# Optimization experiments

Hardware: AMD Instinct MI355X
Metric: run time of the kernel (lower is better)

## Reference

```python
import jax, jax.numpy as jnp
import numpy as np

B, C, L = 128, 12, 1024
N_DIL, DIV, H, K, KSZ, NCP = 7, 2, 32, 8, 9, 6


def setup_inputs() -> dict:
    key = jax.random.key(0)
    kx, kw, ki = jax.random.split(key, 3)
    X = jax.random.normal(kx, (B, C, L), dtype=jnp.float32)
    W = jax.random.normal(kw, (N_DIL, DIV, K * H, 1, KSZ), dtype=jnp.float32)
    # Hydra weight normalization: zero mean, unit L1 norm along the kernel taps
    W = W - W.mean(-1, keepdims=True)
    W = W / jnp.abs(W).sum(-1, keepdims=True)
    I = jax.random.randint(ki, (N_DIL, DIV, H, NCP), 0, C, dtype=jnp.int32)
    return {"X": X, "W": W, "I": I}


def _forward(X, W, I):
    b = X.shape[0]
    diff_X = X[..., 1:] - X[..., :-1]  # first-order difference series
    bi = jnp.arange(b)[:, None, None]
    hi = jnp.arange(H)[None, :, None]
    Z = []
    for di in range(N_DIL):
        d = 2 ** di
        p = (KSZ - 1) * d // 2  # 'same' padding -> output length == input length
        for j in range(DIV):
            src = X if j == 0 else diff_X
            # irregular channel gather + sum over selected channels: [b, H, L']
            g = src[:, I[di, j]].sum(2)
            # grouped dilated conv1d: groups=H, k=K outputs per group -> [b, K*H, L']
            y = jax.lax.conv_general_dilated(
                g, W[di, j], window_strides=(1,), padding=[(p, p)],
                rhs_dilation=(d,), dimension_numbers=("NCH", "OIH", "NCH"),
                feature_group_count=H)
            y = y.reshape(b, H, K, -1)  # [b, H, K, L'] (group-major channel order)
            mx = y.max(2)               # [b, H, L']
            amx = y.argmax(2)
            amn = y.argmin(2)
            # scatter_add histograms over which kernel won at each position
            count_max = jnp.zeros((b, H, K), y.dtype).at[bi, hi, amx].add(mx)
            count_min = jnp.zeros((b, H, K), y.dtype).at[bi, hi, amn].add(jnp.ones_like(mx))
            Z.append(count_max)
            Z.append(count_min)
    return jnp.concatenate(Z, axis=1).reshape(b, -1)


def reference(X, W, I):
    return _forward(X, W, I)
```

## Files before the change

kernel.cpp:

```cpp
#include <hip/hip_runtime.h>

#define NB 128
#define NC 12
#define NL 1024
#define NDIL 7
#define NDIV 2
#define NH 32
#define NK 8
#define NKSZ 9
#define NNCP 6
#define OUTPB (NDIL*NDIV*2*NH*NK)

#define SER_STRIDE 1280
#define LDS_FLOATS (4*SER_STRIDE + 256)

__device__ __forceinline__ float4 ld4(const float* p) { return *(const float4*)p; }

__device__ __forceinline__ float sgpr_f(float v) {
    return __int_as_float(__builtin_amdgcn_readfirstlane(__float_as_int(v)));
}

template<int CTRL, int RM>
__device__ __forceinline__ float dppadd_f(float x) {
    int t = __builtin_amdgcn_update_dpp(0, __float_as_int(x), CTRL, RM, 0xf, false);
    return x + __int_as_float(t);
}
template<int CTRL, int RM>
__device__ __forceinline__ unsigned dppadd_u(unsigned x) {
    int t = __builtin_amdgcn_update_dpp(0, (int)x, CTRL, RM, 0xf, false);
    return x + (unsigned)t;
}
#define RSUM_F(x) { x = dppadd_f<0x111,0xf>(x); x = dppadd_f<0x112,0xf>(x); \
                    x = dppadd_f<0x114,0xf>(x); x = dppadd_f<0x118,0xf>(x); \
                    x = dppadd_f<0x142,0xa>(x); x = dppadd_f<0x143,0xc>(x); }
#define RSUM_U(x) { x = dppadd_u<0x111,0xf>(x); x = dppadd_u<0x112,0xf>(x); \
                    x = dppadd_u<0x114,0xf>(x); x = dppadd_u<0x118,0xf>(x); \
                    x = dppadd_u<0x142,0xa>(x); x = dppadd_u<0x143,0xc>(x); }

#define Wk(k,t) wf[(k)*NKSZ+(t)]

#define ARGBIN(A, OK)                                                     \
    {                                                                     \
        float mx = fmaxf(fmaxf(A[0], A[1]), A[2]);                        \
        mx = fmaxf(fmaxf(mx, A[3]), A[4]);                                \
        mx = fmaxf(fmaxf(mx, A[5]), A[6]);                                \
        mx = fmaxf(mx, A[7]);                                             \
        float mn = fminf(fminf(A[0], A[1]), A[2]);                        \
        mn = fminf(fminf(mn, A[3]), A[4]);                                \
        mn = fminf(fminf(mn, A[5]), A[6]);                                \
        mn = fminf(mn, A[7]);                                             \
        if (OK) {                                                         \
            _Pragma("unroll")                                             \
            for (int k = 0; k < NK; ++k) {                                \
                cm[k] += (A[k] == mx) ? A[k] : 0.f;                       \
                cn[k] += (A[k] == mn) ? 1u : 0u;                          \
            }                                                             \
        }                                                                 \
    }

template<int D>
__device__ __forceinline__ void conv_body(const float* __restrict__ bp0,
                                          const float (&wf)[NK*NKSZ], bool okl,
                                          float (&cm)[NK], unsigned (&cn)[NK]) {
    if constexpr (D == 1) {
        const float* bp = bp0 - 4;
        for (int c = 0; c < 8; ++c, bp += 128) {
            float2 q0 = *(const float2*)(bp);
            float2 q1 = *(const float2*)(bp + 2);
            float2 q2 = *(const float2*)(bp + 4);
            float2 q3 = *(const float2*)(bp + 6);
            float2 q4 = *(const float2*)(bp + 8);
            const float win[10] = { q0.x,q0.y,q1.x,q1.y,q2.x,q2.y,q3.x,q3.y,q4.x,q4.y };
            float a0[NK], a1[NK];
            #pragma unroll
            for (int k = 0; k < NK; ++k) { a0[k] = 0.f; a1[k] = 0.f; }
            #pragma unroll
            for (int t = 0; t < NKSZ; ++t)
                #pragma unroll
                for (int k = 0; k < NK; ++k) {
                    a0[k] = fmaf(Wk(k,t), win[t],   a0[k]);
                    a1[k] = fmaf(Wk(k,t), win[t+1], a1[k]);
                }
            ARGBIN(a0, true);
            ARGBIN(a1, (c != 7) || okl);
        }
    } else {
        const float* bp = bp0 - 4*D;
        for (int c = 0; c < 8; ++c, bp += 128) {
            float2 r[NKSZ];
            #pragma unroll
            for (int t = 0; t < NKSZ; ++t)
                r[t] = *(const float2*)(bp + t*D);
            float a0[NK], a1[NK];
            #pragma unroll
            for (int k = 0; k < NK; ++k) { a0[k] = 0.f; a1[k] = 0.f; }
            #pragma unroll
            for (int t = 0; t < NKSZ; ++t)
                #pragma unroll
                for (int k = 0; k < NK; ++k) {
                    a0[k] = fmaf(Wk(k,t), r[t].x, a0[k]);
                    a1[k] = fmaf(Wk(k,t), r[t].y, a1[k]);
                }
            ARGBIN(a0, true);
            ARGBIN(a1, (c != 7) || okl);
        }
    }
}

__global__ __launch_bounds__(256) void hydra_kernel(
    const float* __restrict__ X,
    const float* __restrict__ W,
    const int*   __restrict__ I,
    float*       __restrict__ out)
{
    __shared__ float lds[LDS_FLOATS];

    const int bid = blockIdx.x;
    const int h4 = bid & 7;
    const int dj = (bid >> 3) % 14;
    const int b  = (bid >> 3) / 14;
    const int di = dj >> 1;
    const int j  = dj & 1;

    const int tid  = threadIdx.x;
    const int lane = tid & 63;
    const int wid  = __builtin_amdgcn_readfirstlane(tid >> 6);
    const int h    = h4 * 4 + wid;
    const int Sw   = 256 + wid * SER_STRIDE;

    #pragma unroll
    for (int z = 0; z < 2; ++z) {
        float4 zz; zz.x = 0.f; zz.y = 0.f; zz.z = 0.f; zz.w = 0.f;
        *(float4*)(lds + (wid + z) * SER_STRIDE + 4 * lane) = zz;
    }

    const int* idx = I + ((di*NDIV + j)*NH + h)*NNCP;
    const float* xb = X + (size_t)b * NC * NL;
    const float* p0 = xb + idx[0]*NL;
    const float* p1 = xb + idx[1]*NL;
    const float* p2 = xb + idx[2]*NL;
    const float* p3 = xb + idx[3]*NL;
    const float* p4 = xb + idx[4]*NL;
    const float* p5 = xb + idx[5]*NL;

    if (j == 0) {
        #pragma unroll
        for (int c = 0; c < 4; ++c) {
            const int e = 256*c + 4*lane;
            float4 v0 = ld4(p0+e), v1 = ld4(p1+e), v2 = ld4(p2+e);
            float4 v3 = ld4(p3+e), v4 = ld4(p4+e), v5 = ld4(p5+e);
            float4 s;
            s.x = v0.x+v1.x+v2.x+v3.x+v4.x+v5.x;
            s.y = v0.y+v1.y+v2.y+v3.y+v4.y+v5.y;
            s.z = v0.z+v1.z+v2.z+v3.z+v4.z+v5.z;
            s.w = v0.w+v1.w+v2.w+v3.w+v4.w+v5.w;
            *(float4*)(lds + Sw + e) = s;
        }
    } else {
        float4 sa[4];
        #pragma unroll
        for (int c = 0; c < 4; ++c) {
            const int e = 256*c + 4*lane;
            float4 v0 = ld4(p0+e), v1 = ld4(p1+e), v2 = ld4(p2+e);
            float4 v3 = ld4(p3+e), v4 = ld4(p4+e), v5 = ld4(p5+e);
            sa[c].x = v0.x+v1.x+v2.x+v3.x+v4.x+v5.x;
            sa[c].y = v0.y+v1.y+v2.y+v3.y+v4.y+v5.y;
            sa[c].z = v0.z+v1.z+v2.z+v3.z+v4.z+v5.z;
            sa[c].w = v0.w+v1.w+v2.w+v3.w+v4.w+v5.w;
        }
        #pragma unroll
        for (int c = 0; c < 4; ++c) {
            const float nxt = (c < 3) ? __shfl(sa[(c+1) & 3].x, 0, 64) : 0.f;
            const float sh  = __shfl_down(sa[c].x, 1, 64);
            const float Se4 = (lane == 63) ? nxt : sh;
            float4 df;
            df.x = sa[c].y - sa[c].x;
            df.y = sa[c].z - sa[c].y;
            df.z = sa[c].w - sa[c].z;
            df.w = Se4 - sa[c].w;
            if (c == 3 && lane == 63) df.w = 0.f;
            const int e = 256*c + 4*lane;
            *(float4*)(lds + Sw + e) = df;
        }
    }

    float wf[NK*NKSZ];
    {
        const float* Wp = W + (size_t)((di*NDIV + j)*(NK*NH) + h*NK) * NKSZ;
        #pragma unroll
        for (int i = 0; i < 18; ++i) {
            float4 v = ld4(Wp + 4*i);
            wf[4*i+0] = sgpr_f(v.x); wf[4*i+1] = sgpr_f(v.y);
            wf[4*i+2] = sgpr_f(v.z); wf[4*i+3] = sgpr_f(v.w);
        }
    }

    float    cm[NK];
    unsigned cn[NK];
    #pragma unroll
    for (int k = 0; k < NK; ++k) { cm[k] = 0.f; cn[k] = 0u; }

    const float* bp0 = lds + Sw + 2*lane;
    const bool   okl = (j == 0) || (lane != 63);

    switch (di) {
        case 0: conv_body<1>( bp0, wf, okl, cm, cn); break;
        case 1: conv_body<2>( bp0, wf, okl, cm, cn); break;
        case 2: conv_body<4>( bp0, wf, okl, cm, cn); break;
        case 3: conv_body<8>( bp0, wf, okl, cm, cn); break;
        case 4: conv_body<16>(bp0, wf, okl, cm, cn); break;
        case 5: conv_body<32>(bp0, wf, okl, cm, cn); break;
        default: conv_body<64>(bp0, wf, okl, cm, cn); break;
    }

    unsigned cp[4];
    #pragma unroll
    for (int i = 0; i < 4; ++i) cp[i] = cn[2*i] | (cn[2*i+1] << 16);

    #pragma unroll
    for (int k = 0; k < NK; ++k) RSUM_F(cm[k]);
    #pragma unroll
    for (int i = 0; i < 4; ++i) RSUM_U(cp[i]);

    if (lane == 63) {
        float* ob = out + (size_t)b*OUTPB + (dj*2)*(NH*NK) + h*NK;
        #pragma unroll
        for (int k = 0; k < NK; ++k) ob[k] = cm[k];
        float* oc = ob + NH*NK;
        #pragma unroll
        for (int i = 0; i < 4; ++i) {
            oc[2*i]     = (float)(cp[i] & 0xffffu);
            oc[2*i + 1] = (float)(cp[i] >> 16);
        }
    }
}

extern "C" void kernel_launch(void* const* d_in, const int* in_sizes, int n_in,
                              void* d_out, int out_size, void* d_ws, size_t ws_size,
                              hipStream_t stream) {
    const float* X = (const float*)d_in[0];
    const float* W = (const float*)d_in[1];
    const int*   I = (const int*)d_in[2];
    float* out = (float*)d_out;

    const int nblocks = NB * (NDIL*NDIV) * (NH/4);
    hydra_kernel<<<dim3(nblocks), dim3(256), 0, stream>>>(X, W, I, out);
}
```

Baseline: 159.1 us.

## Store LDS series as packed fp16 and loop persistent blocks over work items

The gathered channel-sum and difference series are packed to fp16 with round-toward-zero when written to LDS and widened back to fp32 when read for the dilated convolution. This halves LDS footprint and read width. The grid becomes a fixed 2048 blocks, each looping over 7 work items, with a launch-bounds hint for 8 blocks per CU, to cut block launch overhead and raise occupancy. The cost is extra convert instructions. The reduced precision can also flip which kernel wins argmax/argmin, which changes the histogram counts relative to the fp32 reference.

```diff
diff --git a/kernel.cpp b/kernel.cpp
--- a/kernel.cpp
+++ b/kernel.cpp
@@ -11,13 +11,25 @@
 #define NNCP 6
 #define OUTPB (NDIL*NDIV*2*NH*NK)
 
-#define SER_STRIDE 1280
-#define LDS_FLOATS (4*SER_STRIDE + 256)
+#define SER16 1280
+#define LDS_F16 (4*SER16 + 256)
+
+#define GRID_BLOCKS 2048
+#define ITEMS_PER_BLOCK 7
+
+typedef __fp16 h2 __attribute__((ext_vector_type(2)));
 
 __device__ __forceinline__ float4 ld4(const float* p) { return *(const float4*)p; }
 
 __device__ __forceinline__ float sgpr_f(float v) {
     return __int_as_float(__builtin_amdgcn_readfirstlane(__float_as_int(v)));
+}
+__device__ __forceinline__ h2 pkrtz(float x, float y) {
+    return __builtin_amdgcn_cvt_pkrtz(x, y);
+}
+__device__ __forceinline__ float2 cvt2(unsigned u) {
+    h2 v = __builtin_bit_cast(h2, u);
+    float2 r; r.x = (float)v.x; r.y = (float)v.y; return r;
 }
 
 template<int CTRL, int RM>
@@ -59,17 +71,17 @@
     }
 
 template<int D>
-__device__ __forceinline__ void conv_body(const float* __restrict__ bp0,
+__device__ __forceinline__ void conv_body(const __fp16* __restrict__ bp0,
                                           const float (&wf)[NK*NKSZ], bool okl,
                                           float (&cm)[NK], unsigned (&cn)[NK]) {
     if constexpr (D == 1) {
-        const float* bp = bp0 - 4;
+        const __fp16* bp = bp0 - 4;
         for (int c = 0; c < 8; ++c, bp += 128) {
-            float2 q0 = *(const float2*)(bp);
-            float2 q1 = *(const float2*)(bp + 2);
-            float2 q2 = *(const float2*)(bp + 4);
-            float2 q3 = *(const float2*)(bp + 6);
-            float2 q4 = *(const float2*)(bp + 8);
+            float2 q0 = cvt2(*(const unsigned*)(bp));
+            float2 q1 = cvt2(*(const unsigned*)(bp + 2));
+            float2 q2 = cvt2(*(const unsigned*)(bp + 4));
+            float2 q3 = cvt2(*(const unsigned*)(bp + 6));
+            float2 q4 = cvt2(*(const unsigned*)(bp + 8));
             const float win[10] = { q0.x,q0.y,q1.x,q1.y,q2.x,q2.y,q3.x,q3.y,q4.x,q4.y };
             float a0[NK], a1[NK];
             #pragma unroll
@@ -85,12 +97,12 @@
             ARGBIN(a1, (c != 7) || okl);
         }
     } else {
-        const float* bp = bp0 - 4*D;
+        const __fp16* bp = bp0 - 4*D;
         for (int c = 0; c < 8; ++c, bp += 128) {
             float2 r[NKSZ];
             #pragma unroll
             for (int t = 0; t < NKSZ; ++t)
-                r[t] = *(const float2*)(bp + t*D);
+                r[t] = cvt2(*(const unsigned*)(bp + t*D));
             float a0[NK], a1[NK];
             #pragma unroll
             for (int k = 0; k < NK; ++k) { a0[k] = 0.f; a1[k] = 0.f; }
@@ -107,130 +119,139 @@
     }
 }
 
-__global__ __launch_bounds__(256) void hydra_kernel(
+__global__ __launch_bounds__(256, 8) void hydra_kernel(
     const float* __restrict__ X,
     const float* __restrict__ W,
     const int*   __restrict__ I,
     float*       __restrict__ out)
 {
-    __shared__ float lds[LDS_FLOATS];
-
-    const int bid = blockIdx.x;
-    const int h4 = bid & 7;
-    const int dj = (bid >> 3) % 14;
-    const int b  = (bid >> 3) / 14;
-    const int di = dj >> 1;
-    const int j  = dj & 1;
+    __shared__ __fp16 lds16[LDS_F16];
 
     const int tid  = threadIdx.x;
     const int lane = tid & 63;
     const int wid  = __builtin_amdgcn_readfirstlane(tid >> 6);
-    const int h    = h4 * 4 + wid;
-    const int Sw   = 256 + wid * SER_STRIDE;
+    const int Sw   = 256 + wid * SER16;
 
     #pragma unroll
     for (int z = 0; z < 2; ++z) {
-        float4 zz; zz.x = 0.f; zz.y = 0.f; zz.z = 0.f; zz.w = 0.f;
-        *(float4*)(lds + (wid + z) * SER_STRIDE + 4 * lane) = zz;
-    }
-
-    const int* idx = I + ((di*NDIV + j)*NH + h)*NNCP;
-    const float* xb = X + (size_t)b * NC * NL;
-    const float* p0 = xb + idx[0]*NL;
-    const float* p1 = xb + idx[1]*NL;
-    const float* p2 = xb + idx[2]*NL;
-    const float* p3 = xb + idx[3]*NL;
-    const float* p4 = xb + idx[4]*NL;
-    const float* p5 = xb + idx[5]*NL;
-
-    if (j == 0) {
-        #pragma unroll
-        for (int c = 0; c < 4; ++c) {
-            const int e = 256*c + 4*lane;
-            float4 v0 = ld4(p0+e), v1 = ld4(p1+e), v2 = ld4(p2+e);
-            float4 v3 = ld4(p3+e), v4 = ld4(p4+e), v5 = ld4(p5+e);
-            float4 s;
-            s.x = v0.x+v1.x+v2.x+v3.x+v4.x+v5.x;
-            s.y = v0.y+v1.y+v2.y+v3.y+v4.y+v5.y;
-            s.z = v0.z+v1.z+v2.z+v3.z+v4.z+v5.z;
-            s.w = v0.w+v1.w+v2.w+v3.w+v4.w+v5.w;
-            *(float4*)(lds + Sw + e) = s;
-        }
-    } else {
-        float4 sa[4];
-        #pragma unroll
-        for (int c = 0; c < 4; ++c) {
-            const int e = 256*c + 4*lane;
-            float4 v0 = ld4(p0+e), v1 = ld4(p1+e), v2 = ld4(p2+e);
-            float4 v3 = ld4(p3+e), v4 = ld4(p4+e), v5 = ld4(p5+e);
-            sa[c].x = v0.x+v1.x+v2.x+v3.x+v4.x+v5.x;
-            sa[c].y = v0.y+v1.y+v2.y+v3.y+v4.y+v5.y;
-            sa[c].z = v0.z+v1.z+v2.z+v3.z+v4.z+v5.z;
-            sa[c].w = v0.w+v1.w+v2.w+v3.w+v4.w+v5.w;
-        }
-        #pragma unroll
-        for (int c = 0; c < 4; ++c) {
-            const float nxt = (c < 3) ? __shfl(sa[(c+1) & 3].x, 0, 64) : 0.f;
-            const float sh  = __shfl_down(sa[c].x, 1, 64);
-            const float Se4 = (lane == 63) ? nxt : sh;
-            float4 df;
-            df.x = sa[c].y - sa[c].x;
-            df.y = sa[c].z - sa[c].y;
-            df.z = sa[c].w - sa[c].z;
-            df.w = Se4 - sa[c].w;
-            if (c == 3 && lane == 63) df.w = 0.f;
-            const int e = 256*c + 4*lane;
-            *(float4*)(lds + Sw + e) = df;
-        }
-    }
-
-    float wf[NK*NKSZ];
-    {
-        const float* Wp = W + (size_t)((di*NDIV + j)*(NK*NH) + h*NK) * NKSZ;
-        #pragma unroll
-        for (int i = 0; i < 18; ++i) {
-            float4 v = ld4(Wp + 4*i);
-            wf[4*i+0] = sgpr_f(v.x); wf[4*i+1] = sgpr_f(v.y);
-            wf[4*i+2] = sgpr_f(v.z); wf[4*i+3] = sgpr_f(v.w);
-        }
-    }
-
-    float    cm[NK];
-    unsigned cn[NK];
-    #pragma unroll
-    for (int k = 0; k < NK; ++k) { cm[k] = 0.f; cn[k] = 0u; }
-
-    const float* bp0 = lds + Sw + 2*lane;
-    const bool   okl = (j == 0) || (lane != 63);
-
-    switch (di) {
-        case 0: conv_body<1>( bp0, wf, okl, cm, cn); break;
-        case 1: conv_body<2>( bp0, wf, okl, cm, cn); break;
-        case 2: conv_body<4>( bp0, wf, okl, cm, cn); break;
-        case 3: conv_body<8>( bp0, wf, okl, cm, cn); break;
-        case 4: conv_body<16>(bp0, wf, okl, cm, cn); break;
-        case 5: conv_body<32>(bp0, wf, okl, cm, cn); break;
-        default: conv_body<64>(bp0, wf, okl, cm, cn); break;
-    }
-
-    unsigned cp[4];
-    #pragma unroll
-    for (int i = 0; i < 4; ++i) cp[i] = cn[2*i] | (cn[2*i+1] << 16);
-
-    #pragma unroll
-    for (int k = 0; k < NK; ++k) RSUM_F(cm[k]);
-    #pragma unroll
-    for (int i = 0; i < 4; ++i) RSUM_U(cp[i]);
-
-    if (lane == 63) {
-        float* ob = out + (size_t)b*OUTPB + (dj*2)*(NH*NK) + h*NK;
-        #pragma unroll
-        for (int k = 0; k < NK; ++k) ob[k] = cm[k];
-        float* oc = ob + NH*NK;
-        #pragma unroll
-        for (int i = 0; i < 4; ++i) {
-            oc[2*i]     = (float)(cp[i] & 0xffffu);
-            oc[2*i + 1] = (float)(cp[i] >> 16);
+        uint2 zz; zz.x = 0u; zz.y = 0u;
+        *(uint2*)(lds16 + (wid + z) * SER16 + 4 * lane) = zz;
+    }
+
+    #pragma unroll 1
+    for (int it = 0; it < ITEMS_PER_BLOCK; ++it) {
+        const int item = blockIdx.x + it * GRID_BLOCKS;
+        const int h4 = item & 7;
+        const int dj = (item >> 3) % 14;
+        const int b  = (item >> 3) / 14;
+        const int di = dj >> 1;
+        const int j  = dj & 1;
+        const int h  = h4 * 4 + wid;
+
+        const int* idx = I + ((di*NDIV + j)*NH + h)*NNCP;
+        const float* xb = X + (size_t)b * NC * NL;
+        const float* p0 = xb + idx[0]*NL;
+        const float* p1 = xb + idx[1]*NL;
+        const float* p2 = xb + idx[2]*NL;
+        const float* p3 = xb + idx[3]*NL;
+        const float* p4 = xb + idx[4]*NL;
+        const float* p5 = xb + idx[5]*NL;
+
+        if (j == 0) {
+            #pragma unroll
+            for (int c = 0; c < 4; ++c) {
+                const int e = 256*c + 4*lane;
+                float4 v0 = ld4(p0+e), v1 = ld4(p1+e), v2 = ld4(p2+e);
+                float4 v3 = ld4(p3+e), v4 = ld4(p4+e), v5 = ld4(p5+e);
+                float4 s;
+                s.x = v0.x+v1.x+v2.x+v3.x+v4.x+v5.x;
+                s.y = v0.y+v1.y+v2.y+v3.y+v4.y+v5.y;
+                s.z = v0.z+v1.z+v2.z+v3.z+v4.z+v5.z;
+                s.w = v0.w+v1.w+v2.w+v3.w+v4.w+v5.w;
+                uint2 pk;
+                pk.x = __builtin_bit_cast(unsigned, pkrtz(s.x, s.y));
+                pk.y = __builtin_bit_cast(unsigned, pkrtz(s.z, s.w));
+                *(uint2*)(lds16 + Sw + e) = pk;
+            }
+        } else {
+            float4 sa[4];
+            #pragma unroll
+            for (int c = 0; c < 4; ++c) {
+                const int e = 256*c + 4*lane;
+                float4 v0 = ld4(p0+e), v1 = ld4(p1+e), v2 = ld4(p2+e);
+                float4 v3 = ld4(p3+e), v4 = ld4(p4+e), v5 = ld4(p5+e);
+                sa[c].x = v0.x+v1.x+v2.x+v3.x+v4.x+v5.x;
+                sa[c].y = v0.y+v1.y+v2.y+v3.y+v4.y+v5.y;
+                sa[c].z = v0.z+v1.z+v2.z+v3.z+v4.z+v5.z;
+                sa[c].w = v0.w+v1.w+v2.w+v3.w+v4.w+v5.w;
+            }
+            #pragma unroll
+            for (int c = 0; c < 4; ++c) {
+                const float nxt = (c < 3) ? __shfl(sa[(c+1) & 3].x, 0, 64) : 0.f;
+                const float sh  = __shfl_down(sa[c].x, 1, 64);
+                const float Se4 = (lane == 63) ? nxt : sh;
+                float4 df;
+                df.x = sa[c].y - sa[c].x;
+                df.y = sa[c].z - sa[c].y;
+                df.z = sa[c].w - sa[c].z;
+                df.w = Se4 - sa[c].w;
+                if (c == 3 && lane == 63) df.w = 0.f;
+                const int e = 256*c + 4*lane;
+                uint2 pk;
+                pk.x = __builtin_bit_cast(unsigned, pkrtz(df.x, df.y));
+                pk.y = __builtin_bit_cast(unsigned, pkrtz(df.z, df.w));
+                *(uint2*)(lds16 + Sw + e) = pk;
+            }
+        }
+
+        float wf[NK*NKSZ];
+        {
+            const float* Wp = W + (size_t)((di*NDIV + j)*(NK*NH) + h*NK) * NKSZ;
+            #pragma unroll
+            for (int i = 0; i < 18; ++i) {
+                float4 v = ld4(Wp + 4*i);
+                wf[4*i+0] = sgpr_f(v.x); wf[4*i+1] = sgpr_f(v.y);
+                wf[4*i+2] = sgpr_f(v.z); wf[4*i+3] = sgpr_f(v.w);
+            }
+        }
+
+        float    cm[NK];
+        unsigned cn[NK];
+        #pragma unroll
+        for (int k = 0; k < NK; ++k) { cm[k] = 0.f; cn[k] = 0u; }
+
+        const __fp16* bp0 = lds16 + Sw + 2*lane;
+        const bool    okl = (j == 0) || (lane != 63);
+
+        switch (di) {
+            case 0: conv_body<1>( bp0, wf, okl, cm, cn); break;
+            case 1: conv_body<2>( bp0, wf, okl, cm, cn); break;
+            case 2: conv_body<4>( bp0, wf, okl, cm, cn); break;
+            case 3: conv_body<8>( bp0, wf, okl, cm, cn); break;
+            case 4: conv_body<16>(bp0, wf, okl, cm, cn); break;
+            case 5: conv_body<32>(bp0, wf, okl, cm, cn); break;
+            default: conv_body<64>(bp0, wf, okl, cm, cn); break;
+        }
+
+        unsigned cp[4];
+        #pragma unroll
+        for (int i = 0; i < 4; ++i) cp[i] = cn[2*i] | (cn[2*i+1] << 16);
+
+        #pragma unroll
+        for (int k = 0; k < NK; ++k) RSUM_F(cm[k]);
+        #pragma unroll
+        for (int i = 0; i < 4; ++i) RSUM_U(cp[i]);
+
+        if (lane == 63) {
+            float* ob = out + (size_t)b*OUTPB + (dj*2)*(NH*NK) + h*NK;
+            #pragma unroll
+            for (int k = 0; k < NK; ++k) ob[k] = cm[k];
+            float* oc = ob + NH*NK;
+            #pragma unroll
+            for (int i = 0; i < 4; ++i) {
+                oc[2*i]     = (float)(cp[i] & 0xffffu);
+                oc[2*i + 1] = (float)(cp[i] >> 16);
+            }
         }
     }
 }
@@ -243,6 +264,5 @@
     const int*   I = (const int*)d_in[2];
     float* out = (float*)d_out;
 
-    const int nblocks = NB * (NDIL*NDIV) * (NH/4);
-    hydra_kernel<<<dim3(nblocks), dim3(256), 0, stream>>>(X, W, I, out);
-}
+    hydra_kernel<<<dim3(GRID_BLOCKS), dim3(256), 0, stream>>>(X, W, I, out);
+}
```

New measurement: 283.6 us. +78.2%, slower.
